# Optimization experiments

Hardware: AMD Instinct MI355X
Metric: run time of the kernel (lower is better)

The kernel has to match this reference:

```python
import jax, jax.numpy as jnp
import numpy as np

D_MODEL = 1024
NUM_HEADS = 16
D_K = D_MODEL // NUM_HEADS
THETA = 10000.0


def setup_inputs() -> dict:
    key = jax.random.key(0)
    ks = jax.random.split(key, 5)
    B, S = 2, 2048
    sigma = np.sqrt(2.0 / (D_MODEL + D_MODEL))
    x = jax.random.normal(ks[0], (B, S, D_MODEL), dtype=jnp.float32)
    Wq = jax.random.normal(ks[1], (D_MODEL, D_MODEL), dtype=jnp.float32) * sigma
    Wk = jax.random.normal(ks[2], (D_MODEL, D_MODEL), dtype=jnp.float32) * sigma
    Wv = jax.random.normal(ks[3], (D_MODEL, D_MODEL), dtype=jnp.float32) * sigma
    Wo = jax.random.normal(ks[4], (D_MODEL, D_MODEL), dtype=jnp.float32) * sigma
    return {"x": x, "Wq": Wq, "Wk": Wk, "Wv": Wv, "Wo": Wo}


def _rope(x, cos, sin):
    # x: [B, H, S, D_K]; cos/sin: [S, D_K//2] broadcast to [1, 1, S, D_K//2]
    x1 = x[..., ::2]
    x2 = x[..., 1::2]
    even = x1 * cos - x2 * sin
    odd = x1 * sin + x2 * cos
    return jnp.stack((even, odd), axis=-1).reshape(x.shape)


def reference(x, Wq, Wk, Wv, Wo):
    B, S, _ = x.shape
    # projections: weight is (out, in), applied as einsum('oi,...i->...o')
    q = jnp.einsum('oi,bsi->bso', Wq, x).reshape(B, S, NUM_HEADS, D_K).transpose(0, 2, 1, 3)
    k = jnp.einsum('oi,bsi->bso', Wk, x).reshape(B, S, NUM_HEADS, D_K).transpose(0, 2, 1, 3)
    v = jnp.einsum('oi,bsi->bso', Wv, x).reshape(B, S, NUM_HEADS, D_K).transpose(0, 2, 1, 3)
    # RoPE tables (token_positions = arange(S))
    inv_freq = 1.0 / (THETA ** (jnp.arange(0, D_K, 2, dtype=jnp.float32) / D_K))
    t = jnp.arange(S, dtype=jnp.float32)
    freqs = t[:, None] * inv_freq[None, :]          # [S, D_K/2]
    cos = jnp.cos(freqs)[None, None]                # [1,1,S,D_K/2]
    sin = jnp.sin(freqs)[None, None]
    q = _rope(q, cos, sin)
    k = _rope(k, cos, sin)
    # causal attention, full materialized scores (faithful to source)
    scores = jnp.einsum('bhid,bhjd->bhij', q, k) / np.sqrt(D_K).astype(np.float32)
    causal = jnp.tril(jnp.ones((S, S), dtype=bool))
    scores = jnp.where(causal, scores, -jnp.inf)
    attn = jax.nn.softmax(scores, axis=-1)
    out = jnp.einsum('bhij,bhjd->bhid', attn, v)    # [B,H,S,D_K]
    out = out.transpose(0, 2, 1, 3).reshape(B, S, D_MODEL)
    return jnp.einsum('oi,bsi->bso', Wo, out)
```

## Files before the change

kernel.cpp:

```cpp
#include <hip/hip_runtime.h>

#define D_MODEL 1024
#define NUM_HEADS 16
#define SEQ 2048
#define BATCH 2

typedef __attribute__((ext_vector_type(8))) short bf16x8;
typedef __attribute__((ext_vector_type(4))) float f32x4;

__device__ __forceinline__ float bf2f(unsigned short u) {
    return __uint_as_float(((unsigned int)u) << 16);
}
__device__ __forceinline__ unsigned short f2bf(float f) {
    unsigned int u = __float_as_uint(f);
    return (unsigned short)((u + 0x7FFFu + ((u >> 16) & 1u)) >> 16);
}
__device__ __forceinline__ ushort4 pack4(float4 v) {
    return make_ushort4(f2bf(v.x), f2bf(v.y), f2bf(v.z), f2bf(v.w));
}

__device__ __forceinline__ void gload_lds16(const unsigned short* g, unsigned short* l) {
    __builtin_amdgcn_global_load_lds(
        (const __attribute__((address_space(1))) unsigned int*)g,
        (__attribute__((address_space(3))) unsigned int*)l,
        16, 0, 0);
}

__device__ __forceinline__ bf16x8 lds_read_swz(const unsigned short (*tile)[64], int row, int chunk) {
    const char* p = reinterpret_cast<const char*>(tile);
    return *reinterpret_cast<const bf16x8*>(p + row * 128 + (((chunk ^ (row & 7))) << 4));
}

__device__ __forceinline__ bf16x8 lds_read_swz32(const unsigned short (*tile)[32], int row, int chunk) {
    const char* p = reinterpret_cast<const char*>(tile);
    return *reinterpret_cast<const bf16x8*>(p + row * 64 + (((chunk ^ (row & 3))) << 4));
}

__global__ __launch_bounds__(256) void conv_kernel(
    const float* __restrict__ src, unsigned short* __restrict__ dst, int n4)
{
    int i = blockIdx.x * 256 + threadIdx.x;
    if (i < n4) {
        float4 v = reinterpret_cast<const float4*>(src)[i];
        reinterpret_cast<ushort4*>(dst)[i] = pack4(v);
    }
}

__global__ __launch_bounds__(256) void conv4_kernel(
    const float* __restrict__ x, const float* __restrict__ Wq,
    const float* __restrict__ Wk, const float* __restrict__ Wv,
    unsigned short* __restrict__ xb, unsigned short* __restrict__ w3bf,
    float2* __restrict__ tab)
{
    int i = blockIdx.x * 256 + threadIdx.x;
    if (i < 1835008) {
        const float* src;
        unsigned short* dst;
        int off;
        if (i < 1048576) {
            src = x; dst = xb; off = i;
        } else {
            int j = i - 1048576;
            int which = j >> 18;
            off = j & 0x3FFFF;
            src = (which == 0) ? Wq : (which == 1) ? Wk : Wv;
            dst = w3bf + ((size_t)which << 20);
        }
        float4 v = reinterpret_cast<const float4*>(src)[off];
        reinterpret_cast<ushort4*>(dst)[off] = pack4(v);
    } else {
        int idx = i - 1835008;
        int s = idx >> 5, d2 = idx & 31;
        float inv = powf(10000.0f, -(float)d2 / 32.0f);
        float sn, cs;
        sincosf((float)s * inv, &sn, &cs);
        tab[idx] = make_float2(cs, sn);
    }
}

__global__ __launch_bounds__(256) void qkv_mfma_kernel(
    const unsigned short* __restrict__ xb,
    const unsigned short* __restrict__ w3,
    const float2* __restrict__ tab,
    unsigned short* __restrict__ qb, unsigned short* __restrict__ kb,
    unsigned short* __restrict__ vt)
{
    const int lin = blockIdx.x;
    const int b = lin & 7;
    const int t = lin >> 3;
    const int which = t % 3;
    const int y = t / 3;
    const unsigned short* __restrict__ W = w3 + (size_t)which * 1048576;
    const int m0 = y * 128;
    const int n0g = b * 128;

    __shared__ __align__(16) unsigned short As[2][128][32];
    __shared__ __align__(16) unsigned short Bs[2][128][32];

    const int tid = threadIdx.x;
    const int w = tid >> 6;
    const int lane = tid & 63;
    const int quad = lane >> 4;
    const int c15 = lane & 15;
    const int qm = w >> 1, qn = w & 1;
    const int srow4 = lane >> 2;
    const int sch4 = lane & 3;

    auto stage = [&](int k0, int buf) {
#pragma unroll
        for (int i = 0; i < 2; i++) {
            const int row = i * 64 + w * 16 + srow4;
            const int ch = sch4 ^ (row & 3);
            gload_lds16(xb + (size_t)(m0 + row) * 1024 + k0 + ch * 8,
                        &As[buf][i * 64 + w * 16][0]);
            gload_lds16(W + (size_t)(n0g + row) * 1024 + k0 + ch * 8,
                        &Bs[buf][i * 64 + w * 16][0]);
        }
    };

    f32x4 acc[4][4];
#pragma unroll
    for (int mi = 0; mi < 4; mi++)
#pragma unroll
        for (int ni = 0; ni < 4; ni++) acc[mi][ni] = (f32x4){0.f, 0.f, 0.f, 0.f};

    stage(0, 0);
    for (int k0 = 0; k0 < 1024; k0 += 32) {
        const int cb = (k0 >> 5) & 1;
        __syncthreads();
        if (k0 < 992) stage(k0 + 32, cb ^ 1);

        bf16x8 af[4], bfr[4];
#pragma unroll
        for (int mi = 0; mi < 4; mi++)
            af[mi] = lds_read_swz32(As[cb], qm * 64 + mi * 16 + c15, quad);
#pragma unroll
        for (int ni = 0; ni < 4; ni++)
            bfr[ni] = lds_read_swz32(Bs[cb], qn * 64 + ni * 16 + c15, quad);
#pragma unroll
        for (int mi = 0; mi < 4; mi++)
#pragma unroll
            for (int ni = 0; ni < 4; ni++)
                acc[mi][ni] = __builtin_amdgcn_mfma_f32_16x16x32_bf16(af[mi], bfr[ni], acc[mi][ni], 0, 0, 0);
    }

    __syncthreads();
    unsigned short* stg = &As[0][0][0] + w * (16 * 72);
    const int hq = b * 2 + qn;
    unsigned short* outp = (which == 0) ? qb : kb;
    const int odd = c15 & 1;

#pragma unroll
    for (int mi = 0; mi < 4; mi++) {
#pragma unroll
        for (int r = 0; r < 4; r++) {
            int m = m0 + qm * 64 + mi * 16 + quad * 4 + r;
            int s = m & (SEQ - 1);
            const float2* trow = tab + (s << 5);
#pragma unroll
            for (int ni = 0; ni < 4; ni++) {
                float val = acc[mi][ni][r];
                float res;
                if (which < 2) {
                    float part = __shfl_xor(val, 1);
                    float2 cs = trow[(ni * 16 + c15) >> 1];
                    res = odd ? (part * cs.y + val * cs.x) : (val * cs.x - part * cs.y);
                } else {
                    res = val;
                }
                stg[(quad * 4 + r) * 72 + ni * 16 + c15] = f2bf(res);
            }
        }
        if (which < 2) {
            int row = lane >> 2;
            int ch = lane & 3;
            int m = m0 + qm * 64 + mi * 16 + row;
            int s = m & (SEQ - 1);
            int bb = m >> 11;
            size_t ob = (((size_t)bb * NUM_HEADS + hq) * SEQ + s) * 64 + ch * 16;
            uint4 v0 = *reinterpret_cast<const uint4*>(&stg[row * 72 + ch * 16]);
            uint4 v1 = *reinterpret_cast<const uint4*>(&stg[row * 72 + ch * 16 + 8]);
            *reinterpret_cast<uint4*>(&outp[ob]) = v0;
            *reinterpret_cast<uint4*>(&outp[ob + 8]) = v1;
        } else {
            int mbase = m0 + qm * 64 + mi * 16;
            int bb = mbase >> 11;
            int s_base = mbase & (SEQ - 1);
            unsigned short tmp[16];
#pragma unroll
            for (int sl = 0; sl < 16; sl++) tmp[sl] = stg[sl * 72 + lane];
            size_t ob = (((size_t)bb * NUM_HEADS + hq) * 64 + lane) * SEQ + s_base;
            *reinterpret_cast<uint4*>(&vt[ob])     = *reinterpret_cast<uint4*>(&tmp[0]);
            *reinterpret_cast<uint4*>(&vt[ob + 8]) = *reinterpret_cast<uint4*>(&tmp[8]);
        }
    }
}

__global__ __launch_bounds__(256) void attn_kernel(
    const unsigned short* __restrict__ qb, const unsigned short* __restrict__ kb,
    const unsigned short* __restrict__ vt, unsigned short* __restrict__ ab)
{
    const int xpair = blockIdx.x;
    const int bh = blockIdx.y;
    const int b = bh >> 4, h = bh & 15;
    const size_t base = (size_t)bh * SEQ * 64;
    const size_t vbase = (size_t)bh * 64 * SEQ;
    const int tid = threadIdx.x;
    const int w = tid >> 6;
    const int lane = tid & 63;
    const int quad = lane >> 4;
    const int c15 = lane & 15;
    const int srow8 = lane >> 3;
    const int sch = lane & 7;
    const float C = 0.125f;

    __shared__ __align__(16) unsigned short Ks[2][64][64];
    __shared__ __align__(16) unsigned short Vs[2][64][64];
    __shared__ __align__(16) unsigned short Pl[64][72];

    auto stage = [&](int jts, int buf) {
        const int j0s = jts * 64;
#pragma unroll
        for (int i = 0; i < 2; i++) {
            const int row = w * 16 + i * 8 + srow8;
            const int ch = sch ^ (row & 7);
            gload_lds16(kb + base + (size_t)(j0s + row) * 64 + ch * 8,
                        &Ks[buf][w * 16 + i * 8][0]);
            gload_lds16(vt + vbase + (size_t)row * SEQ + j0s + ch * 8,
                        &Vs[buf][w * 16 + i * 8][0]);
        }
    };

    for (int pass = 0; pass < 2; pass++) {
        const int it = pass ? xpair : (31 - xpair);
        const int i0 = it * 64;

        const int qrow = i0 + w * 16 + c15;
        bf16x8 qf0 = *reinterpret_cast<const bf16x8*>(&qb[base + (size_t)qrow * 64 + quad * 8]);
        bf16x8 qf1 = *reinterpret_cast<const bf16x8*>(&qb[base + (size_t)qrow * 64 + 32 + quad * 8]);

        float m_st = -1e30f, l_st = 0.f;
        f32x4 Oc[4];
#pragma unroll
        for (int t = 0; t < 4; t++) Oc[t] = (f32x4){0.f, 0.f, 0.f, 0.f};

        __syncthreads();
        stage(0, 0);

        for (int jt = 0; jt <= it; jt++) {
            const int j0 = jt * 64;
            const int cb = jt & 1;

            __syncthreads();
            if (jt < it) stage(jt + 1, cb ^ 1);

            bf16x8 kc0[4], kc1[4];
#pragma unroll
            for (int t = 0; t < 4; t++) {
                kc0[t] = lds_read_swz(Ks[cb], t * 16 + c15, quad);
                kc1[t] = lds_read_swz(Ks[cb], t * 16 + c15, 4 + quad);
            }

            f32x4 sc[4];
#pragma unroll
            for (int t = 0; t < 4; t++) sc[t] = (f32x4){0.f, 0.f, 0.f, 0.f};
#pragma unroll
            for (int t = 0; t < 4; t++) {
                sc[t] = __builtin_amdgcn_mfma_f32_16x16x32_bf16(kc0[t], qf0, sc[t], 0, 0, 0);
                sc[t] = __builtin_amdgcn_mfma_f32_16x16x32_bf16(kc1[t], qf1, sc[t], 0, 0, 0);
            }

            bf16x8 vv0[4], vv1[4];
#pragma unroll
            for (int t = 0; t < 4; t++) {
                vv0[t] = lds_read_swz(Vs[cb], t * 16 + c15, quad);
                vv1[t] = lds_read_swz(Vs[cb], t * 16 + c15, 4 + quad);
            }

            if (jt == it) {
                const int gi = i0 + w * 16 + c15;
#pragma unroll
                for (int t = 0; t < 4; t++) {
#pragma unroll
                    for (int r = 0; r < 4; r++) {
                        int gj = j0 + t * 16 + quad * 4 + r;
                        if (gj > gi) sc[t][r] = -1e30f;
                    }
                }
            }

            float x0 = fmaxf(fmaxf(sc[0][0], sc[0][1]), fmaxf(sc[0][2], sc[0][3]));
            float x1 = fmaxf(fmaxf(sc[1][0], sc[1][1]), fmaxf(sc[1][2], sc[1][3]));
            float x2 = fmaxf(fmaxf(sc[2][0], sc[2][1]), fmaxf(sc[2][2], sc[2][3]));
            float x3 = fmaxf(fmaxf(sc[3][0], sc[3][1]), fmaxf(sc[3][2], sc[3][3]));
            float tm = fmaxf(fmaxf(x0, x1), fmaxf(x2, x3));
            tm = fmaxf(tm, __shfl_xor(tm, 16));
            tm = fmaxf(tm, __shfl_xor(tm, 32));

            if (!__all(tm <= m_st + 64.0f)) {
                float mnew = fmaxf(m_st, tm);
                float alpha = __expf((m_st - mnew) * C);
                l_st *= alpha;
#pragma unroll
                for (int t = 0; t < 4; t++)
#pragma unroll
                    for (int r = 0; r < 4; r++) Oc[t][r] *= alpha;
                m_st = mnew;
            }

            const float mC = m_st * C;
            float p[4][4];
#pragma unroll
            for (int t = 0; t < 4; t++)
#pragma unroll
                for (int r = 0; r < 4; r++)
                    p[t][r] = __expf(__builtin_fmaf(sc[t][r], C, -mC));

            float s0 = (p[0][0] + p[0][1]) + (p[0][2] + p[0][3]);
            float s1 = (p[1][0] + p[1][1]) + (p[1][2] + p[1][3]);
            float s2 = (p[2][0] + p[2][1]) + (p[2][2] + p[2][3]);
            float s3 = (p[3][0] + p[3][1]) + (p[3][2] + p[3][3]);
            l_st += (s0 + s1) + (s2 + s3);

#pragma unroll
            for (int t = 0; t < 4; t++) {
#pragma unroll
                for (int hh = 0; hh < 2; hh++) {
                    unsigned int pk = (unsigned int)f2bf(p[t][2 * hh])
                                    | ((unsigned int)f2bf(p[t][2 * hh + 1]) << 16);
                    *reinterpret_cast<unsigned int*>(
                        &Pl[w * 16 + c15][t * 16 + quad * 4 + 2 * hh]) = pk;
                }
            }

            bf16x8 ap0 = *reinterpret_cast<const bf16x8*>(&Pl[w * 16 + c15][quad * 8]);
            bf16x8 ap1 = *reinterpret_cast<const bf16x8*>(&Pl[w * 16 + c15][32 + quad * 8]);
#pragma unroll
            for (int t = 0; t < 4; t++) {
                Oc[t] = __builtin_amdgcn_mfma_f32_16x16x32_bf16(vv0[t], ap0, Oc[t], 0, 0, 0);
                Oc[t] = __builtin_amdgcn_mfma_f32_16x16x32_bf16(vv1[t], ap1, Oc[t], 0, 0, 0);
            }
        }

        l_st += __shfl_xor(l_st, 16);
        l_st += __shfl_xor(l_st, 32);
        float inv = 1.0f / l_st;
#pragma unroll
        for (int t = 0; t < 4; t++) {
#pragma unroll
            for (int hh = 0; hh < 2; hh++) {
                unsigned int pk = (unsigned int)f2bf(Oc[t][2 * hh] * inv)
                                | ((unsigned int)f2bf(Oc[t][2 * hh + 1] * inv) << 16);
                *reinterpret_cast<unsigned int*>(
                    &Pl[w * 16 + c15][t * 16 + quad * 4 + 2 * hh]) = pk;
            }
        }
        {
            int row = lane >> 2;
            int ch = lane & 3;
            int gi = i0 + w * 16 + row;
            size_t ob = ((size_t)b * SEQ + gi) * 1024 + h * 64 + ch * 16;
            uint4 v0 = *reinterpret_cast<const uint4*>(&Pl[w * 16 + row][ch * 16]);
            uint4 v1 = *reinterpret_cast<const uint4*>(&Pl[w * 16 + row][ch * 16 + 8]);
            *reinterpret_cast<uint4*>(&ab[ob]) = v0;
            *reinterpret_cast<uint4*>(&ab[ob + 8]) = v1;
        }
    }
}

__global__ __launch_bounds__(256) void out_mfma_kernel(
    const unsigned short* __restrict__ A, const unsigned short* __restrict__ Wob,
    float* __restrict__ out)
{
    const int lin = blockIdx.x;
    const int b = lin & 7;
    const int y = lin >> 3;
    const int m0 = y * 64;
    const int n0g = b * 128;

    __shared__ __align__(16) unsigned short As[2][64][32];
    __shared__ __align__(16) unsigned short Bs[2][128][32];

    const int tid = threadIdx.x;
    const int w = tid >> 6;
    const int lane = tid & 63;
    const int quad = lane >> 4;
    const int c15 = lane & 15;
    const int qm = w >> 1, qn = w & 1;
    const int srow4 = lane >> 2;
    const int sch4 = lane & 3;

    auto stage = [&](int k0, int buf) {
        {
            const int row = w * 16 + srow4;
            const int ch = sch4 ^ (row & 3);
            gload_lds16(A + (size_t)(m0 + row) * 1024 + k0 + ch * 8,
                        &As[buf][w * 16][0]);
        }
#pragma unroll
        for (int i = 0; i < 2; i++) {
            const int row = i * 64 + w * 16 + srow4;
            const int ch = sch4 ^ (row & 3);
            gload_lds16(Wob + (size_t)(n0g + row) * 1024 + k0 + ch * 8,
                        &Bs[buf][i * 64 + w * 16][0]);
        }
    };

    f32x4 acc[2][4];
#pragma unroll
    for (int mi = 0; mi < 2; mi++)
#pragma unroll
        for (int ni = 0; ni < 4; ni++) acc[mi][ni] = (f32x4){0.f, 0.f, 0.f, 0.f};

    stage(0, 0);
    for (int k0 = 0; k0 < 1024; k0 += 32) {
        const int cb = (k0 >> 5) & 1;
        __syncthreads();
        if (k0 < 992) stage(k0 + 32, cb ^ 1);

        bf16x8 af[2], bfr[4];
#pragma unroll
        for (int mi = 0; mi < 2; mi++)
            af[mi] = lds_read_swz32(As[cb], qm * 32 + mi * 16 + c15, quad);
#pragma unroll
        for (int ni = 0; ni < 4; ni++)
            bfr[ni] = lds_read_swz32(Bs[cb], qn * 64 + ni * 16 + c15, quad);
#pragma unroll
        for (int mi = 0; mi < 2; mi++)
#pragma unroll
            for (int ni = 0; ni < 4; ni++)
                acc[mi][ni] = __builtin_amdgcn_mfma_f32_16x16x32_bf16(af[mi], bfr[ni], acc[mi][ni], 0, 0, 0);
    }

#pragma unroll
    for (int mi = 0; mi < 2; mi++) {
#pragma unroll
        for (int r = 0; r < 4; r++) {
            int m = m0 + qm * 32 + mi * 16 + quad * 4 + r;
#pragma unroll
            for (int ni = 0; ni < 4; ni++) {
                int n = n0g + qn * 64 + ni * 16 + c15;
                out[(size_t)m * 1024 + n] = acc[mi][ni][r];
            }
        }
    }
}

extern "C" void kernel_launch(void* const* d_in, const int* in_sizes, int n_in,
                              void* d_out, int out_size, void* d_ws, size_t ws_size,
                              hipStream_t stream)
{
    const float* x  = (const float*)d_in[0];
    const float* Wq = (const float*)d_in[1];
    const float* Wk = (const float*)d_in[2];
    const float* Wv = (const float*)d_in[3];
    const float* Wo = (const float*)d_in[4];
    float* out = (float*)d_out;

    const size_t QKV_ELEMS = (size_t)BATCH * SEQ * D_MODEL;

    unsigned short* qb = (unsigned short*)d_ws;
    unsigned short* kb = qb + QKV_ELEMS;
    unsigned short* vt = kb + QKV_ELEMS;
    unsigned short* ab = vt + QKV_ELEMS;
    unsigned short* w3bf = ab;
    unsigned short* wobf = qb;
    unsigned short* xbuf = (unsigned short*)d_out;
    float2* tab = (float2*)((char*)d_out + 8 * 1024 * 1024);

    conv4_kernel<<<dim3(7424), 256, 0, stream>>>(x, Wq, Wk, Wv, xbuf, w3bf, tab);
    qkv_mfma_kernel<<<dim3(768), 256, 0, stream>>>(xbuf, w3bf, tab, qb, kb, vt);
    attn_kernel<<<dim3(16, 32), 256, 0, stream>>>(qb, kb, vt, ab);
    conv_kernel<<<dim3(1024), 256, 0, stream>>>(Wo, wobf, 262144);
    out_mfma_kernel<<<dim3(512), 256, 0, stream>>>(ab, wobf, out);
}
```

Baseline: 205.2 us.

## Stage 128-key K/V tiles per barrier and raise MFMA wave priority

The attention kernel now stages K/V in 128-key superblocks, twice as deep as before, with a 16-chunk swizzle for the wider V tile. Each staged block is processed as two 64-key halves, and the half past the diagonal is skipped. This halves the number of __syncthreads barriers and async-load rounds per query tile. MFMA sections are also wrapped in s_setprio to favour matrix issue. In exchange, shared memory doubles to about 73 KB per block, which may reduce occupancy, and the last superblock can load keys that are never used.

```diff
diff --git a/kernel.cpp b/kernel.cpp
--- a/kernel.cpp
+++ b/kernel.cpp
@@ -34,6 +34,11 @@
 __device__ __forceinline__ bf16x8 lds_read_swz32(const unsigned short (*tile)[32], int row, int chunk) {
     const char* p = reinterpret_cast<const char*>(tile);
     return *reinterpret_cast<const bf16x8*>(p + row * 64 + (((chunk ^ (row & 3))) << 4));
+}
+
+__device__ __forceinline__ bf16x8 lds_read_swz128(const unsigned short (*tile)[128], int row, int chunk) {
+    const char* p = reinterpret_cast<const char*>(tile);
+    return *reinterpret_cast<const bf16x8*>(p + row * 256 + (((chunk ^ (row & 15))) << 4));
 }
 
 __global__ __launch_bounds__(256) void conv_kernel(
@@ -212,28 +217,33 @@
     const int c15 = lane & 15;
     const int srow8 = lane >> 3;
     const int sch = lane & 7;
+    const int srow16 = lane >> 4;
+    const int sch16 = lane & 15;
     const float C = 0.125f;
 
-    __shared__ __align__(16) unsigned short Ks[2][64][64];
-    __shared__ __align__(16) unsigned short Vs[2][64][64];
+    __shared__ __align__(16) unsigned short Ks[2][128][64];
+    __shared__ __align__(16) unsigned short Vs[2][64][128];
     __shared__ __align__(16) unsigned short Pl[64][72];
 
-    auto stage = [&](int jts, int buf) {
-        const int j0s = jts * 64;
-#pragma unroll
-        for (int i = 0; i < 2; i++) {
-            const int row = w * 16 + i * 8 + srow8;
-            const int ch = sch ^ (row & 7);
-            gload_lds16(kb + base + (size_t)(j0s + row) * 64 + ch * 8,
-                        &Ks[buf][w * 16 + i * 8][0]);
-            gload_lds16(vt + vbase + (size_t)row * SEQ + j0s + ch * 8,
-                        &Vs[buf][w * 16 + i * 8][0]);
+    auto stage = [&](int sj, int buf) {
+        const int j0s = sj * 128;
+#pragma unroll
+        for (int i = 0; i < 4; i++) {
+            const int krow = w * 32 + i * 8 + srow8;
+            const int kch = sch ^ (krow & 7);
+            gload_lds16(kb + base + (size_t)(j0s + krow) * 64 + kch * 8,
+                        &Ks[buf][w * 32 + i * 8][0]);
+            const int vrow = w * 16 + i * 4 + srow16;
+            const int vch = sch16 ^ (vrow & 15);
+            gload_lds16(vt + vbase + (size_t)vrow * SEQ + j0s + vch * 8,
+                        &Vs[buf][w * 16 + i * 4][0]);
         }
     };
 
     for (int pass = 0; pass < 2; pass++) {
         const int it = pass ? xpair : (31 - xpair);
         const int i0 = it * 64;
+        const int nj = (it >> 1) + 1;
 
         const int qrow = i0 + w * 16 + c15;
         bf16x8 qf0 = *reinterpret_cast<const bf16x8*>(&qb[base + (size_t)qrow * 64 + quad * 8]);
@@ -247,98 +257,107 @@
         __syncthreads();
         stage(0, 0);
 
-        for (int jt = 0; jt <= it; jt++) {
-            const int j0 = jt * 64;
-            const int cb = jt & 1;
+        for (int sj = 0; sj < nj; sj++) {
+            const int cb = sj & 1;
 
             __syncthreads();
-            if (jt < it) stage(jt + 1, cb ^ 1);
-
-            bf16x8 kc0[4], kc1[4];
-#pragma unroll
-            for (int t = 0; t < 4; t++) {
-                kc0[t] = lds_read_swz(Ks[cb], t * 16 + c15, quad);
-                kc1[t] = lds_read_swz(Ks[cb], t * 16 + c15, 4 + quad);
-            }
-
-            f32x4 sc[4];
-#pragma unroll
-            for (int t = 0; t < 4; t++) sc[t] = (f32x4){0.f, 0.f, 0.f, 0.f};
-#pragma unroll
-            for (int t = 0; t < 4; t++) {
-                sc[t] = __builtin_amdgcn_mfma_f32_16x16x32_bf16(kc0[t], qf0, sc[t], 0, 0, 0);
-                sc[t] = __builtin_amdgcn_mfma_f32_16x16x32_bf16(kc1[t], qf1, sc[t], 0, 0, 0);
-            }
-
-            bf16x8 vv0[4], vv1[4];
-#pragma unroll
-            for (int t = 0; t < 4; t++) {
-                vv0[t] = lds_read_swz(Vs[cb], t * 16 + c15, quad);
-                vv1[t] = lds_read_swz(Vs[cb], t * 16 + c15, 4 + quad);
-            }
-
-            if (jt == it) {
-                const int gi = i0 + w * 16 + c15;
+            if (sj < nj - 1) stage(sj + 1, cb ^ 1);
+
+#pragma unroll
+            for (int hf = 0; hf < 2; hf++) {
+                const int j0 = sj * 128 + hf * 64;
+                if (j0 > i0) continue;
+
+                bf16x8 kc0[4], kc1[4];
 #pragma unroll
                 for (int t = 0; t < 4; t++) {
-#pragma unroll
-                    for (int r = 0; r < 4; r++) {
-                        int gj = j0 + t * 16 + quad * 4 + r;
-                        if (gj > gi) sc[t][r] = -1e30f;
+                    kc0[t] = lds_read_swz(Ks[cb], hf * 64 + t * 16 + c15, quad);
+                    kc1[t] = lds_read_swz(Ks[cb], hf * 64 + t * 16 + c15, 4 + quad);
+                }
+
+                f32x4 sc[4];
+#pragma unroll
+                for (int t = 0; t < 4; t++) sc[t] = (f32x4){0.f, 0.f, 0.f, 0.f};
+                __builtin_amdgcn_s_setprio(1);
+#pragma unroll
+                for (int t = 0; t < 4; t++) {
+                    sc[t] = __builtin_amdgcn_mfma_f32_16x16x32_bf16(kc0[t], qf0, sc[t], 0, 0, 0);
+                    sc[t] = __builtin_amdgcn_mfma_f32_16x16x32_bf16(kc1[t], qf1, sc[t], 0, 0, 0);
+                }
+                __builtin_amdgcn_s_setprio(0);
+
+                bf16x8 vv0[4], vv1[4];
+#pragma unroll
+                for (int t = 0; t < 4; t++) {
+                    vv0[t] = lds_read_swz128(Vs[cb], t * 16 + c15, hf * 8 + quad);
+                    vv1[t] = lds_read_swz128(Vs[cb], t * 16 + c15, hf * 8 + 4 + quad);
+                }
+
+                if (j0 == i0) {
+                    const int gi = i0 + w * 16 + c15;
+#pragma unroll
+                    for (int t = 0; t < 4; t++) {
+#pragma unroll
+                        for (int r = 0; r < 4; r++) {
+                            int gj = j0 + t * 16 + quad * 4 + r;
+                            if (gj > gi) sc[t][r] = -1e30f;
+                        }
                     }
                 }
-            }
-
-            float x0 = fmaxf(fmaxf(sc[0][0], sc[0][1]), fmaxf(sc[0][2], sc[0][3]));
-            float x1 = fmaxf(fmaxf(sc[1][0], sc[1][1]), fmaxf(sc[1][2], sc[1][3]));
-            float x2 = fmaxf(fmaxf(sc[2][0], sc[2][1]), fmaxf(sc[2][2], sc[2][3]));
-            float x3 = fmaxf(fmaxf(sc[3][0], sc[3][1]), fmaxf(sc[3][2], sc[3][3]));
-            float tm = fmaxf(fmaxf(x0, x1), fmaxf(x2, x3));
-            tm = fmaxf(tm, __shfl_xor(tm, 16));
-            tm = fmaxf(tm, __shfl_xor(tm, 32));
-
-            if (!__all(tm <= m_st + 64.0f)) {
-                float mnew = fmaxf(m_st, tm);
-                float alpha = __expf((m_st - mnew) * C);
-                l_st *= alpha;
+
+                float x0 = fmaxf(fmaxf(sc[0][0], sc[0][1]), fmaxf(sc[0][2], sc[0][3]));
+                float x1 = fmaxf(fmaxf(sc[1][0], sc[1][1]), fmaxf(sc[1][2], sc[1][3]));
+                float x2 = fmaxf(fmaxf(sc[2][0], sc[2][1]), fmaxf(sc[2][2], sc[2][3]));
+                float x3 = fmaxf(fmaxf(sc[3][0], sc[3][1]), fmaxf(sc[3][2], sc[3][3]));
+                float tm = fmaxf(fmaxf(x0, x1), fmaxf(x2, x3));
+                tm = fmaxf(tm, __shfl_xor(tm, 16));
+                tm = fmaxf(tm, __shfl_xor(tm, 32));
+
+                if (!__all(tm <= m_st + 64.0f)) {
+                    float mnew = fmaxf(m_st, tm);
+                    float alpha = __expf((m_st - mnew) * C);
+                    l_st *= alpha;
+#pragma unroll
+                    for (int t = 0; t < 4; t++)
+#pragma unroll
+                        for (int r = 0; r < 4; r++) Oc[t][r] *= alpha;
+                    m_st = mnew;
+                }
+
+                const float mC = m_st * C;
+                float p[4][4];
 #pragma unroll
                 for (int t = 0; t < 4; t++)
 #pragma unroll
-                    for (int r = 0; r < 4; r++) Oc[t][r] *= alpha;
-                m_st = mnew;
-            }
-
-            const float mC = m_st * C;
-            float p[4][4];
-#pragma unroll
-            for (int t = 0; t < 4; t++)
-#pragma unroll
-                for (int r = 0; r < 4; r++)
-                    p[t][r] = __expf(__builtin_fmaf(sc[t][r], C, -mC));
-
-            float s0 = (p[0][0] + p[0][1]) + (p[0][2] + p[0][3]);
-            float s1 = (p[1][0] + p[1][1]) + (p[1][2] + p[1][3]);
-            float s2 = (p[2][0] + p[2][1]) + (p[2][2] + p[2][3]);
-            float s3 = (p[3][0] + p[3][1]) + (p[3][2] + p[3][3]);
-            l_st += (s0 + s1) + (s2 + s3);
-
-#pragma unroll
-            for (int t = 0; t < 4; t++) {
-#pragma unroll
-                for (int hh = 0; hh < 2; hh++) {
-                    unsigned int pk = (unsigned int)f2bf(p[t][2 * hh])
-                                    | ((unsigned int)f2bf(p[t][2 * hh + 1]) << 16);
-                    *reinterpret_cast<unsigned int*>(
-                        &Pl[w * 16 + c15][t * 16 + quad * 4 + 2 * hh]) = pk;
-                }
-            }
-
-            bf16x8 ap0 = *reinterpret_cast<const bf16x8*>(&Pl[w * 16 + c15][quad * 8]);
-            bf16x8 ap1 = *reinterpret_cast<const bf16x8*>(&Pl[w * 16 + c15][32 + quad * 8]);
-#pragma unroll
-            for (int t = 0; t < 4; t++) {
-                Oc[t] = __builtin_amdgcn_mfma_f32_16x16x32_bf16(vv0[t], ap0, Oc[t], 0, 0, 0);
-                Oc[t] = __builtin_amdgcn_mfma_f32_16x16x32_bf16(vv1[t], ap1, Oc[t], 0, 0, 0);
+                    for (int r = 0; r < 4; r++)
+                        p[t][r] = __expf(__builtin_fmaf(sc[t][r], C, -mC));
+
+                float s0 = (p[0][0] + p[0][1]) + (p[0][2] + p[0][3]);
+                float s1 = (p[1][0] + p[1][1]) + (p[1][2] + p[1][3]);
+                float s2 = (p[2][0] + p[2][1]) + (p[2][2] + p[2][3]);
+                float s3 = (p[3][0] + p[3][1]) + (p[3][2] + p[3][3]);
+                l_st += (s0 + s1) + (s2 + s3);
+
+#pragma unroll
+                for (int t = 0; t < 4; t++) {
+#pragma unroll
+                    for (int hh = 0; hh < 2; hh++) {
+                        unsigned int pk = (unsigned int)f2bf(p[t][2 * hh])
+                                        | ((unsigned int)f2bf(p[t][2 * hh + 1]) << 16);
+                        *reinterpret_cast<unsigned int*>(
+                            &Pl[w * 16 + c15][t * 16 + quad * 4 + 2 * hh]) = pk;
+                    }
+                }
+
+                bf16x8 ap0 = *reinterpret_cast<const bf16x8*>(&Pl[w * 16 + c15][quad * 8]);
+                bf16x8 ap1 = *reinterpret_cast<const bf16x8*>(&Pl[w * 16 + c15][32 + quad * 8]);
+                __builtin_amdgcn_s_setprio(1);
+#pragma unroll
+                for (int t = 0; t < 4; t++) {
+                    Oc[t] = __builtin_amdgcn_mfma_f32_16x16x32_bf16(vv0[t], ap0, Oc[t], 0, 0, 0);
+                    Oc[t] = __builtin_amdgcn_mfma_f32_16x16x32_bf16(vv1[t], ap1, Oc[t], 0, 0, 0);
+                }
+                __builtin_amdgcn_s_setprio(0);
             }
         }
 
```

New measurement: 202.3 us. No clear change (-1.4%).
